# Performance work log

Measured on AMD Instinct MI355X. Metric: run time of the kernel, lower is better.

## Reference

```python
import jax, jax.numpy as jnp
import numpy as np

N_HEADS = 8
HEAD_DIM = 64  # hidden_dim 512 / 8 heads
EPS = 1e-12    # F.normalize clamp_min eps


def setup_inputs() -> dict:
    key = jax.random.key(0)
    k1, k2, k3, k4 = jax.random.split(key, 4)
    B, C, H, W = 2, 256, 48, 48
    hidden = N_HEADS * HEAD_DIM
    x = jax.random.normal(k1, (B, C, H, W), dtype=jnp.float32)
    w_qkv = jax.random.normal(k2, (hidden * 3, C), dtype=jnp.float32) * 0.02
    w_proj = jax.random.normal(k3, (C, hidden), dtype=jnp.float32) * 0.02
    b_proj = jax.random.normal(k4, (C,), dtype=jnp.float32) * 0.02
    return {"x": x, "w_qkv": w_qkv, "w_proj": w_proj, "b_proj": b_proj}


def _l2norm_tokens(t):
    # normalize along the token axis (last dim), matching F.normalize(dim=-1)
    n = jnp.sqrt(jnp.sum(t * t, axis=-1, keepdims=True))
    return t / jnp.maximum(n, EPS)


def reference(x, w_qkv, w_proj, b_proj):
    B, C, H, W = x.shape
    N = H * W
    # 1x1 conv == channel matmul
    qkv = jnp.einsum('oc,bchw->bohw', w_qkv, x)  # [B, 3*hidden, H, W]
    qkv = qkv.reshape(B, 3, N_HEADS, HEAD_DIM, N)
    q, k, v = qkv[:, 0], qkv[:, 1], qkv[:, 2]    # each [B, h, d, N]
    q = _l2norm_tokens(q)
    k = _l2norm_tokens(k)
    # attn = q^T @ k over head_dim -> [B, h, N, N]; note: qk_scale unused in source
    attn = jnp.einsum('bhdn,bhdm->bhnm', q, k)
    attn = jax.nn.softmax(attn, axis=-1)
    # out = attn @ v^T -> [B, h, N, d], then permute to [B, h, d, N]
    out = jnp.einsum('bhnm,bhdm->bhdn', attn, v)
    out = out.reshape(B, N_HEADS * HEAD_DIM, H, W)
    # proj 1x1 conv with bias
    y = jnp.einsum('oc,bchw->bohw', w_proj, out) + b_proj[None, :, None, None]
    return y
```

## Files before the change

### kernel.cpp

```cpp
#include <hip/hip_runtime.h>
#include <math.h>

#define NTOK 2304
#define BATCH 2
#define CIN 256
#define HID 512
#define NH 8
#define LOG2E 1.44269504088896340736f

typedef __attribute__((ext_vector_type(8))) short bfrag;
typedef __attribute__((ext_vector_type(16))) float f32x16;

#if __has_builtin(__builtin_amdgcn_exp2f)
#define EXP2(x) __builtin_amdgcn_exp2f(x)
#else
#define EXP2(x) exp2f(x)
#endif

__device__ __forceinline__ unsigned f2bf(float f) {
    unsigned u = __float_as_uint(f);
    u += 0x7FFF + ((u >> 16) & 1);
    return u >> 16;
}

__device__ __forceinline__ unsigned pk_trunc(float a, float b) {
    return __builtin_amdgcn_perm(__float_as_uint(b), __float_as_uint(a), 0x07060302u);
}

__device__ __forceinline__ void softmax_frag(
    const f32x16& accS, int h, float& ps0, float& ps1, bfrag& P0, bfrag& P1)
{
    unsigned dw[8];
#pragma unroll
    for (int i = 0; i < 8; i++) {
        float plo = EXP2(accS[2 * i]);
        float phi = EXP2(accS[2 * i + 1]);
        dw[i] = pk_trunc(plo, phi);
        ps0 += __uint_as_float(dw[i] << 16);
        ps1 += __uint_as_float(dw[i] & 0xffff0000u);
    }
    unsigned sa0 = h ? dw[0] : dw[2], sb0 = h ? dw[1] : dw[3];
    unsigned sa1 = h ? dw[4] : dw[6], sb1 = h ? dw[5] : dw[7];
    unsigned ra0 = (unsigned)__shfl_xor((int)sa0, 32, 64);
    unsigned rb0 = (unsigned)__shfl_xor((int)sb0, 32, 64);
    unsigned ra1 = (unsigned)__shfl_xor((int)sa1, 32, 64);
    unsigned rb1 = (unsigned)__shfl_xor((int)sb1, 32, 64);
    union { bfrag f; unsigned u[4]; } U0, U1;
    U0.u[0] = h ? ra0 : dw[0];  U0.u[1] = h ? rb0 : dw[1];
    U0.u[2] = h ? dw[2] : ra0;  U0.u[3] = h ? dw[3] : rb0;
    U1.u[0] = h ? ra1 : dw[4];  U1.u[1] = h ? rb1 : dw[5];
    U1.u[2] = h ? dw[6] : ra1;  U1.u[3] = h ? dw[7] : rb1;
    P0 = U0.f; P1 = U1.f;
}

__global__ __launch_bounds__(256) void pack_weights(
    const float* __restrict__ wq, short* __restrict__ wqb,
    const float* __restrict__ wp, short* __restrict__ wpb)
{
    int e = (blockIdx.x * 256 + threadIdx.x) * 8;
    const int NQ = 1536 * 256;
    const float* src; short* dst;
    if (e < NQ) {
        int row = e >> 8, c = e & 255;
        int off = (((row >> 5) * 16 + (c >> 4)) * 64 + ((c >> 3) & 1) * 32 + (row & 31)) * 8;
        src = wq + e; dst = wqb + off;
    } else {
        int e2 = e - NQ;
        int row = e2 >> 9, c = e2 & 511;
        int off = (((row >> 5) * 32 + (c >> 4)) * 64 + ((c >> 3) & 1) * 32 + (row & 31)) * 8;
        src = wp + e2; dst = wpb + off;
    }
    float4 v0 = ((const float4*)src)[0];
    float4 v1 = ((const float4*)src)[1];
    unsigned b0 = f2bf(v0.x) | (f2bf(v0.y) << 16);
    unsigned b1 = f2bf(v0.z) | (f2bf(v0.w) << 16);
    unsigned b2 = f2bf(v1.x) | (f2bf(v1.y) << 16);
    unsigned b3 = f2bf(v1.z) | (f2bf(v1.w) << 16);
    *((uint4*)dst) = make_uint4(b0, b1, b2, b3);
}

__global__ __launch_bounds__(256) void pack_xT(
    const float* __restrict__ x, short* __restrict__ xT)
{
    int n0 = blockIdx.x * 64, c0 = blockIdx.y * 64, b = blockIdx.z;
    __shared__ float sT[64][65];
    int tid = threadIdx.x, lane = tid & 63, wv = tid >> 6;
    for (int c = wv; c < 64; c += 4)
        sT[c][lane] = x[((size_t)b * CIN + c0 + c) * NTOK + n0 + lane];
    __syncthreads();
    int n = tid >> 2, c4 = (tid & 3) * 16;
    unsigned buf[8];
#pragma unroll
    for (int i = 0; i < 8; i++)
        buf[i] = f2bf(sT[c4 + 2 * i][n]) | (f2bf(sT[c4 + 2 * i + 1][n]) << 16);
    int n_tok = n0 + n;
    int l31n = n & 31;
    short* dst = xT + (((size_t)b * 72 + (n_tok >> 5)) * 16 + ((c0 + c4) >> 4)) * 512;
    ((uint4*)(dst + (0 * 32 + l31n) * 8))[0] = make_uint4(buf[0], buf[1], buf[2], buf[3]);
    ((uint4*)(dst + (1 * 32 + l31n) * 8))[0] = make_uint4(buf[4], buf[5], buf[6], buf[7]);
}

__global__ __launch_bounds__(256, 2) void gemm_qkv(
    const short* __restrict__ A,
    const short* __restrict__ B,
    float* __restrict__ qkf, short* __restrict__ vb)
{
    int b = blockIdx.z;
    int o0 = blockIdx.y * 128;
    int n0 = blockIdx.x * 128;
    int tid = threadIdx.x, wv = tid >> 6, lane = tid & 63;
    int h = lane >> 5, l31 = lane & 31;

    const short* pa = A + ((size_t)(o0 >> 5) * 16) * 512 + lane * 8;
    const short* pb = B + (((size_t)b * 72 + (n0 >> 5) + wv) * 16) * 512 + lane * 8;

    f32x16 acc[4];
#pragma unroll
    for (int rb = 0; rb < 4; rb++)
#pragma unroll
        for (int r = 0; r < 16; r++) acc[rb][r] = 0.f;

#pragma unroll 2
    for (int kc = 0; kc < 16; kc++) {
        bfrag a0 = *(const bfrag*)(pa + (size_t)(0 * 16 + kc) * 512);
        bfrag a1 = *(const bfrag*)(pa + (size_t)(1 * 16 + kc) * 512);
        bfrag a2 = *(const bfrag*)(pa + (size_t)(2 * 16 + kc) * 512);
        bfrag a3 = *(const bfrag*)(pa + (size_t)(3 * 16 + kc) * 512);
        bfrag bb = *(const bfrag*)(pb + (size_t)kc * 512);
        acc[0] = __builtin_amdgcn_mfma_f32_32x32x16_bf16(a0, bb, acc[0], 0, 0, 0);
        acc[1] = __builtin_amdgcn_mfma_f32_32x32x16_bf16(a1, bb, acc[1], 0, 0, 0);
        acc[2] = __builtin_amdgcn_mfma_f32_32x32x16_bf16(a2, bb, acc[2], 0, 0, 0);
        acc[3] = __builtin_amdgcn_mfma_f32_32x32x16_bf16(a3, bb, acc[3], 0, 0, 0);
    }

    int nn = n0 + wv * 32 + l31;
    if (o0 < 1024) {
        float* Q = qkf + (size_t)b * 1024 * NTOK;
#pragma unroll
        for (int rb = 0; rb < 4; rb++)
#pragma unroll
            for (int r = 0; r < 16; r++) {
                int ml = (r & 3) + 8 * (r >> 2) + 4 * h;
                Q[(size_t)(o0 + rb * 32 + ml) * NTOK + nn] = acc[rb][r];
            }
    } else {
        short* V = vb + (size_t)b * 512 * NTOK;
        int ov = o0 - 1024;
        int mb = nn >> 5, jc = (nn >> 4) & 1, hv = (nn >> 3) & 1, e = nn & 7;
#pragma unroll
        for (int rb = 0; rb < 4; rb++)
#pragma unroll
            for (int r = 0; r < 16; r++) {
                int ml = (r & 3) + 8 * (r >> 2) + 4 * h;
                int row = ov + rb * 32 + ml;
                int hh2 = row >> 6, dl = row & 63;
                int jr = dl >> 5, l31v = dl & 31;
                V[((((size_t)hh2 * 72 + mb) * 4 + jr * 2 + jc) * 64
                   + hv * 32 + l31v) * 8 + e] = (short)f2bf(acc[rb][r]);
            }
    }
}

__global__ __launch_bounds__(256) void rownorm(
    const float* __restrict__ qkf, float* __restrict__ invn)
{
    int row = blockIdx.x;
    int b = row >> 10, o = row & 1023;
    const float* p = qkf + ((size_t)b * 1024 + o) * NTOK;
    int tid = threadIdx.x;
    float s = 0.f;
    for (int n = tid; n < NTOK; n += 256) { float v = p[n]; s += v * v; }
#pragma unroll
    for (int off = 32; off > 0; off >>= 1) s += __shfl_down(s, off, 64);
    __shared__ float ws[4];
    if ((tid & 63) == 0) ws[tid >> 6] = s;
    __syncthreads();
    if (tid == 0) {
        float tot = ws[0] + ws[1] + ws[2] + ws[3];
        invn[row] = 1.f / fmaxf(sqrtf(tot), 1e-12f);
    }
}

__global__ __launch_bounds__(256) void pack_qk(
    const float* __restrict__ qkf, const float* __restrict__ invn,
    short* __restrict__ qkt)
{
    int n0 = blockIdx.x * 64;
    int bh = blockIdx.y;
    int sel = blockIdx.z;
    int b = bh >> 3, h = bh & 7;
    const float* src = qkf + ((size_t)b * 1024 + sel * 512 + h * 64) * NTOK;
    int base = b * 1024 + sel * 512 + h * 64;
    float extra = sel == 0 ? LOG2E : 1.f;

    __shared__ float sT[64][65];
    int tid = threadIdx.x, lane = tid & 63, wv = tid >> 6;
    for (int d = wv; d < 64; d += 4)
        sT[d][lane] = src[(size_t)d * NTOK + n0 + lane] * (invn[base + d] * extra);
    __syncthreads();

    int n = tid >> 2, c4 = (tid & 3) * 16;
    unsigned buf[8];
#pragma unroll
    for (int i = 0; i < 8; i++)
        buf[i] = f2bf(sT[c4 + 2 * i][n]) | (f2bf(sT[c4 + 2 * i + 1][n]) << 16);
    int t = n0 + n;
    int mb = t >> 5, l31 = t & 31, fi = c4 >> 4;
    short* dst = qkt + (size_t)sel * ((size_t)16 * NTOK * 64)
               + (size_t)bh * NTOK * 64
               + ((size_t)mb * 4 + fi) * 512;
    ((uint4*)(dst + (0 * 32 + l31) * 8))[0] = make_uint4(buf[0], buf[1], buf[2], buf[3]);
    ((uint4*)(dst + (1 * 32 + l31) * 8))[0] = make_uint4(buf[4], buf[5], buf[6], buf[7]);
}

__global__ __launch_bounds__(256, 4) void attn_nb(
    const short* __restrict__ qkt,
    const short* __restrict__ vb,
    float* __restrict__ Opart,
    float* __restrict__ lsum)
{
    int bid = blockIdx.x;
    int g = bid & 31;
    int bh = g >> 1, ms = g & 1;
    int ntile = bid >> 5;
    int b = bh >> 3, hh = bh & 7;
    int tid = threadIdx.x, wv = tid >> 6, lane = tid & 63;
    int h = lane >> 5, l31 = lane & 31;
    int nb = ntile * 128 + wv * 32;
    int mb0 = ms * 36;

    const short* Qt = qkt + (size_t)bh * NTOK * 64;
    const short* kp = qkt + (size_t)16 * NTOK * 64 + (size_t)bh * NTOK * 64
                    + ((size_t)mb0 * 4) * 512 + lane * 8;
    const short* vp = vb + (((size_t)(b * 8 + hh) * 72 + mb0) * 4) * 512 + lane * 8;

    bfrag bQ[4];
    {
        const short* q0 = Qt + ((size_t)(nb >> 5) * 4) * 512 + lane * 8;
#pragma unroll
        for (int i = 0; i < 4; i++) bQ[i] = *(const bfrag*)(q0 + i * 512);
    }

    f32x16 aL, aH;
#pragma unroll
    for (int r = 0; r < 16; r++) { aL[r] = 0.f; aH[r] = 0.f; }
    float s0 = 0.f, s1 = 0.f;

    bfrag ck[4], cv[4];
#pragma unroll
    for (int i = 0; i < 4; i++) {
        ck[i] = *(const bfrag*)(kp + i * 512);
        cv[i] = *(const bfrag*)(vp + i * 512);
    }

#pragma unroll 2
    for (int it = 0; it < 36; it++) {
        kp += 2048; vp += 2048;
        bfrag nk[4], nv[4];
#pragma unroll
        for (int i = 0; i < 4; i++) {
            nk[i] = *(const bfrag*)(kp + i * 512);
            nv[i] = *(const bfrag*)(vp + i * 512);
        }

        bfrag P0, P1;
        {
            f32x16 accS;
#pragma unroll
            for (int r = 0; r < 16; r++) accS[r] = 0.f;
            accS = __builtin_amdgcn_mfma_f32_32x32x16_bf16(ck[0], bQ[0], accS, 0, 0, 0);
            accS = __builtin_amdgcn_mfma_f32_32x32x16_bf16(ck[1], bQ[1], accS, 0, 0, 0);
            accS = __builtin_amdgcn_mfma_f32_32x32x16_bf16(ck[2], bQ[2], accS, 0, 0, 0);
            accS = __builtin_amdgcn_mfma_f32_32x32x16_bf16(ck[3], bQ[3], accS, 0, 0, 0);
            softmax_frag(accS, h, s0, s1, P0, P1);
        }
        aL = __builtin_amdgcn_mfma_f32_32x32x16_bf16(P0, cv[0], aL, 0, 0, 0);
        aL = __builtin_amdgcn_mfma_f32_32x32x16_bf16(P1, cv[1], aL, 0, 0, 0);
        aH = __builtin_amdgcn_mfma_f32_32x32x16_bf16(P0, cv[2], aH, 0, 0, 0);
        aH = __builtin_amdgcn_mfma_f32_32x32x16_bf16(P1, cv[3], aH, 0, 0, 0);

#pragma unroll
        for (int i = 0; i < 4; i++) { ck[i] = nk[i]; cv[i] = nv[i]; }
    }

    float p0 = s0 + s1;
    p0 += __shfl_xor(p0, 32, 64);
    if (h == 0)
        lsum[((size_t)ms * 16 + bh) * NTOK + nb + l31] = p0;

    float* Ob = Opart + (size_t)ms * (2ull * NTOK * HID)
              + (size_t)b * NTOK * HID + hh * 64;
#pragma unroll
    for (int r = 0; r < 16; r++) {
        int ml = (r & 3) + 8 * (r >> 2) + 4 * h;
        Ob[(size_t)(nb + ml) * HID + l31] = aL[r];
        Ob[(size_t)(nb + ml) * HID + 32 + l31] = aH[r];
    }
}

__global__ __launch_bounds__(256) void combine(
    const float* __restrict__ Opart, const float* __restrict__ lsum,
    short* __restrict__ aoT)
{
    int s = blockIdx.x * 256 + threadIdx.x;
    int lane = s & 63, kc = (s >> 6) & 31, nbb = s >> 11;
    int b = nbb >= 72 ? 1 : 0, nb = nbb - 72 * b;
    int h = lane >> 5, l31 = lane & 31;
    int n = nb * 32 + l31;
    int k0 = kc * 16 + h * 8;
    int hh = kc >> 2;
    float l0 = lsum[(size_t)(b * 8 + hh) * NTOK + n];
    float l1 = lsum[(size_t)16 * NTOK + (size_t)(b * 8 + hh) * NTOK + n];
    float inv = 1.f / (l0 + l1);
    const float* P0 = Opart + ((size_t)b * NTOK + n) * HID + k0;
    const float* P1 = P0 + (size_t)2 * NTOK * HID;
    float4 a0 = ((const float4*)P0)[0], a1 = ((const float4*)P0)[1];
    float4 c0 = ((const float4*)P1)[0], c1 = ((const float4*)P1)[1];
    unsigned b0 = f2bf((a0.x + c0.x) * inv) | (f2bf((a0.y + c0.y) * inv) << 16);
    unsigned b1 = f2bf((a0.z + c0.z) * inv) | (f2bf((a0.w + c0.w) * inv) << 16);
    unsigned b2 = f2bf((a1.x + c1.x) * inv) | (f2bf((a1.y + c1.y) * inv) << 16);
    unsigned b3 = f2bf((a1.z + c1.z) * inv) | (f2bf((a1.w + c1.w) * inv) << 16);
    *((uint4*)(aoT + (size_t)s * 8)) = make_uint4(b0, b1, b2, b3);
}

__global__ __launch_bounds__(256, 2) void gemm_proj(
    const short* __restrict__ A,
    const short* __restrict__ B,
    const float* __restrict__ bias, float* __restrict__ y)
{
    int b = blockIdx.z;
    int o0 = blockIdx.y * 64;
    int n0 = blockIdx.x * 128;
    int tid = threadIdx.x, wv = tid >> 6, lane = tid & 63;
    int h = lane >> 5, l31 = lane & 31;

    const short* pa = A + ((size_t)(o0 >> 5) * 32) * 512 + lane * 8;
    const short* pb = B + (((size_t)b * 72 + (n0 >> 5) + wv) * 32) * 512 + lane * 8;

    f32x16 acc0, acc1;
#pragma unroll
    for (int r = 0; r < 16; r++) { acc0[r] = 0.f; acc1[r] = 0.f; }

#pragma unroll 4
    for (int kc = 0; kc < 32; kc++) {
        bfrag a0 = *(const bfrag*)(pa + (size_t)kc * 512);
        bfrag a1 = *(const bfrag*)(pa + (size_t)(32 + kc) * 512);
        bfrag bb = *(const bfrag*)(pb + (size_t)kc * 512);
        acc0 = __builtin_amdgcn_mfma_f32_32x32x16_bf16(a0, bb, acc0, 0, 0, 0);
        acc1 = __builtin_amdgcn_mfma_f32_32x32x16_bf16(a1, bb, acc1, 0, 0, 0);
    }

    int nn = n0 + wv * 32 + l31;
#pragma unroll
    for (int r = 0; r < 16; r++) {
        int ml = (r & 3) + 8 * (r >> 2) + 4 * h;
        y[((size_t)b * CIN + o0 + ml) * NTOK + nn] = acc0[r] + bias[o0 + ml];
        y[((size_t)b * CIN + o0 + 32 + ml) * NTOK + nn] = acc1[r] + bias[o0 + 32 + ml];
    }
}

extern "C" void kernel_launch(void* const* d_in, const int* in_sizes, int n_in,
                              void* d_out, int out_size, void* d_ws, size_t ws_size,
                              hipStream_t stream)
{
    const float* x      = (const float*)d_in[0];
    const float* w_qkv  = (const float*)d_in[1];
    const float* w_proj = (const float*)d_in[2];
    const float* b_proj = (const float*)d_in[3];
    float* y = (float*)d_out;

    float* qkf   = (float*)d_ws;
    float* Opart = (float*)d_ws;
    short* vb    = (short*)((char*)d_ws + 18874368);
    short* qkt   = (short*)((char*)d_ws + 23592960);
    short* aoT   = (short*)((char*)d_ws + 23592960);
    float* lsum  = (float*)((char*)d_ws + 33030144);
    short* xT    = (short*)((char*)d_ws + 33030144);
    short* wqb   = (short*)((char*)d_ws + 35389440);
    short* wpb   = (short*)((char*)d_ws + 36175872);
    float* invn  = (float*)((char*)d_ws + 36438016);

    pack_weights<<<(1536 * 256 + 256 * 512) / 8 / 256, 256, 0, stream>>>(
        w_qkv, wqb, w_proj, wpb);
    pack_xT<<<dim3(NTOK / 64, CIN / 64, BATCH), 256, 0, stream>>>(x, xT);
    gemm_qkv<<<dim3(NTOK / 128, 1536 / 128, BATCH), 256, 0, stream>>>(
        wqb, xT, qkf, vb);
    rownorm<<<2048, 256, 0, stream>>>(qkf, invn);
    pack_qk<<<dim3(NTOK / 64, BATCH * NH, 2), 256, 0, stream>>>(qkf, invn, qkt);
    attn_nb<<<576, 256, 0, stream>>>(qkt, vb, Opart, lsum);
    combine<<<1152, 256, 0, stream>>>(Opart, lsum, aoT);
    gemm_proj<<<dim3(NTOK / 128, CIN / 64, BATCH), 256, 0, stream>>>(
        wpb, aoT, b_proj, y);
}
```

Baseline: 147.5 us.

## Fuse QK norm into GEMM epilogue, split attention keys 4-way with bf16 partials

The QKV GEMM now writes Q/K straight into the packed bf16 attention layout and accumulates per-row sum of squares with atomics. This replaces the fp32 qkf round trip and the separate rownorm and pack_qk kernels with a lightweight in-place scale_qk pass. Attention now splits the key range four ways instead of two, doubling the grid to 1152 blocks. Partial outputs are stored as bf16, which halves partial traffic but costs precision, and combine sums four partials. The trade-offs are atomic contention, a double bf16 rounding on Q/K, and bf16 partial sums.

```diff
diff --git a/kernel.cpp b/kernel.cpp
--- a/kernel.cpp
+++ b/kernel.cpp
@@ -55,8 +55,13 @@
 
 __global__ __launch_bounds__(256) void pack_weights(
     const float* __restrict__ wq, short* __restrict__ wqb,
-    const float* __restrict__ wp, short* __restrict__ wpb)
-{
+    const float* __restrict__ wp, short* __restrict__ wpb,
+    float* __restrict__ sumsq)
+{
+    if (blockIdx.x == 0) {
+        ((float4*)sumsq)[threadIdx.x * 2] = make_float4(0.f, 0.f, 0.f, 0.f);
+        ((float4*)sumsq)[threadIdx.x * 2 + 1] = make_float4(0.f, 0.f, 0.f, 0.f);
+    }
     int e = (blockIdx.x * 256 + threadIdx.x) * 8;
     const int NQ = 1536 * 256;
     const float* src; short* dst;
@@ -103,7 +108,9 @@
 __global__ __launch_bounds__(256, 2) void gemm_qkv(
     const short* __restrict__ A,
     const short* __restrict__ B,
-    float* __restrict__ qkf, short* __restrict__ vb)
+    short* __restrict__ qku,
+    short* __restrict__ vb,
+    float* __restrict__ sumsq)
 {
     int b = blockIdx.z;
     int o0 = blockIdx.y * 128;
@@ -135,13 +142,26 @@
 
     int nn = n0 + wv * 32 + l31;
     if (o0 < 1024) {
-        float* Q = qkf + (size_t)b * 1024 * NTOK;
+        int sel = o0 >> 9;
+        short* Qb = qku + (size_t)sel * (16 * NTOK * 64);
+        int mbase = (nn >> 5) * 4, tl = nn & 31;
 #pragma unroll
         for (int rb = 0; rb < 4; rb++)
 #pragma unroll
             for (int r = 0; r < 16; r++) {
                 int ml = (r & 3) + 8 * (r >> 2) + 4 * h;
-                Q[(size_t)(o0 + rb * 32 + ml) * NTOK + nn] = acc[rb][r];
+                int o = o0 + rb * 32 + ml;
+                int hh2 = (o >> 6) & 7, d = o & 63;
+                float v = acc[rb][r];
+                float sq = v * v;
+#pragma unroll
+                for (int off = 1; off < 32; off <<= 1)
+                    sq += __shfl_xor(sq, off, 64);
+                if (l31 == 0)
+                    atomicAdd(sumsq + b * 1024 + o, sq);
+                Qb[(size_t)(b * 8 + hh2) * (NTOK * 64)
+                   + (size_t)(mbase + (d >> 4)) * 512
+                   + (((d >> 3) & 1) * 32 + tl) * 8 + (d & 7)] = (short)f2bf(v);
             }
     } else {
         short* V = vb + (size_t)b * 512 * NTOK;
@@ -161,73 +181,56 @@
     }
 }
 
-__global__ __launch_bounds__(256) void rownorm(
-    const float* __restrict__ qkf, float* __restrict__ invn)
-{
-    int row = blockIdx.x;
-    int b = row >> 10, o = row & 1023;
-    const float* p = qkf + ((size_t)b * 1024 + o) * NTOK;
-    int tid = threadIdx.x;
-    float s = 0.f;
-    for (int n = tid; n < NTOK; n += 256) { float v = p[n]; s += v * v; }
-#pragma unroll
-    for (int off = 32; off > 0; off >>= 1) s += __shfl_down(s, off, 64);
-    __shared__ float ws[4];
-    if ((tid & 63) == 0) ws[tid >> 6] = s;
-    __syncthreads();
-    if (tid == 0) {
-        float tot = ws[0] + ws[1] + ws[2] + ws[3];
-        invn[row] = 1.f / fmaxf(sqrtf(tot), 1e-12f);
-    }
-}
-
-__global__ __launch_bounds__(256) void pack_qk(
-    const float* __restrict__ qkf, const float* __restrict__ invn,
-    short* __restrict__ qkt)
-{
-    int n0 = blockIdx.x * 64;
-    int bh = blockIdx.y;
-    int sel = blockIdx.z;
-    int b = bh >> 3, h = bh & 7;
-    const float* src = qkf + ((size_t)b * 1024 + sel * 512 + h * 64) * NTOK;
-    int base = b * 1024 + sel * 512 + h * 64;
-    float extra = sel == 0 ? LOG2E : 1.f;
-
-    __shared__ float sT[64][65];
-    int tid = threadIdx.x, lane = tid & 63, wv = tid >> 6;
-    for (int d = wv; d < 64; d += 4)
-        sT[d][lane] = src[(size_t)d * NTOK + n0 + lane] * (invn[base + d] * extra);
-    __syncthreads();
-
-    int n = tid >> 2, c4 = (tid & 3) * 16;
-    unsigned buf[8];
-#pragma unroll
-    for (int i = 0; i < 8; i++)
-        buf[i] = f2bf(sT[c4 + 2 * i][n]) | (f2bf(sT[c4 + 2 * i + 1][n]) << 16);
-    int t = n0 + n;
-    int mb = t >> 5, l31 = t & 31, fi = c4 >> 4;
-    short* dst = qkt + (size_t)sel * ((size_t)16 * NTOK * 64)
-               + (size_t)bh * NTOK * 64
-               + ((size_t)mb * 4 + fi) * 512;
-    ((uint4*)(dst + (0 * 32 + l31) * 8))[0] = make_uint4(buf[0], buf[1], buf[2], buf[3]);
-    ((uint4*)(dst + (1 * 32 + l31) * 8))[0] = make_uint4(buf[4], buf[5], buf[6], buf[7]);
+__global__ __launch_bounds__(256) void scale_qk(
+    short* __restrict__ qkt, const float* __restrict__ sumsq)
+{
+    int s = blockIdx.x * 256 + threadIdx.x;
+    int lane = s & 63;
+    int rest = s >> 6;
+    int fi = rest & 3;
+    int selbh = rest / 288;
+    int sel = selbh >> 4, bh = selbh & 15;
+    int b = bh >> 3, hh = bh & 7;
+    int d0 = fi * 16 + (lane >> 5) * 8;
+    const float* sp = sumsq + b * 1024 + sel * 512 + hh * 64 + d0;
+    float scl = sel == 0 ? LOG2E : 1.f;
+    float4 s0 = ((const float4*)sp)[0];
+    float4 s1 = ((const float4*)sp)[1];
+    float i0 = scl / fmaxf(sqrtf(s0.x), 1e-12f);
+    float i1 = scl / fmaxf(sqrtf(s0.y), 1e-12f);
+    float i2 = scl / fmaxf(sqrtf(s0.z), 1e-12f);
+    float i3 = scl / fmaxf(sqrtf(s0.w), 1e-12f);
+    float i4 = scl / fmaxf(sqrtf(s1.x), 1e-12f);
+    float i5 = scl / fmaxf(sqrtf(s1.y), 1e-12f);
+    float i6 = scl / fmaxf(sqrtf(s1.z), 1e-12f);
+    float i7 = scl / fmaxf(sqrtf(s1.w), 1e-12f);
+    uint4 v = ((uint4*)qkt)[s];
+    unsigned o0w = f2bf(__uint_as_float(v.x << 16) * i0)
+                 | (f2bf(__uint_as_float(v.x & 0xffff0000u) * i1) << 16);
+    unsigned o1w = f2bf(__uint_as_float(v.y << 16) * i2)
+                 | (f2bf(__uint_as_float(v.y & 0xffff0000u) * i3) << 16);
+    unsigned o2w = f2bf(__uint_as_float(v.z << 16) * i4)
+                 | (f2bf(__uint_as_float(v.z & 0xffff0000u) * i5) << 16);
+    unsigned o3w = f2bf(__uint_as_float(v.w << 16) * i6)
+                 | (f2bf(__uint_as_float(v.w & 0xffff0000u) * i7) << 16);
+    ((uint4*)qkt)[s] = make_uint4(o0w, o1w, o2w, o3w);
 }
 
 __global__ __launch_bounds__(256, 4) void attn_nb(
     const short* __restrict__ qkt,
     const short* __restrict__ vb,
-    float* __restrict__ Opart,
+    short* __restrict__ Opart,
     float* __restrict__ lsum)
 {
     int bid = blockIdx.x;
-    int g = bid & 31;
-    int bh = g >> 1, ms = g & 1;
-    int ntile = bid >> 5;
+    int g = bid & 63;
+    int bh = g >> 2, ms = g & 3;
+    int ntile = bid >> 6;
     int b = bh >> 3, hh = bh & 7;
     int tid = threadIdx.x, wv = tid >> 6, lane = tid & 63;
     int h = lane >> 5, l31 = lane & 31;
     int nb = ntile * 128 + wv * 32;
-    int mb0 = ms * 36;
+    int mb0 = ms * 18;
 
     const short* Qt = qkt + (size_t)bh * NTOK * 64;
     const short* kp = qkt + (size_t)16 * NTOK * 64 + (size_t)bh * NTOK * 64
@@ -254,7 +257,7 @@
     }
 
 #pragma unroll 2
-    for (int it = 0; it < 36; it++) {
+    for (int it = 0; it < 18; it++) {
         kp += 2048; vp += 2048;
         bfrag nk[4], nv[4];
 #pragma unroll
@@ -288,18 +291,18 @@
     if (h == 0)
         lsum[((size_t)ms * 16 + bh) * NTOK + nb + l31] = p0;
 
-    float* Ob = Opart + (size_t)ms * (2ull * NTOK * HID)
+    short* Ob = Opart + (size_t)ms * (2ull * NTOK * HID)
               + (size_t)b * NTOK * HID + hh * 64;
 #pragma unroll
     for (int r = 0; r < 16; r++) {
         int ml = (r & 3) + 8 * (r >> 2) + 4 * h;
-        Ob[(size_t)(nb + ml) * HID + l31] = aL[r];
-        Ob[(size_t)(nb + ml) * HID + 32 + l31] = aH[r];
+        Ob[(size_t)(nb + ml) * HID + l31] = (short)f2bf(aL[r]);
+        Ob[(size_t)(nb + ml) * HID + 32 + l31] = (short)f2bf(aH[r]);
     }
 }
 
 __global__ __launch_bounds__(256) void combine(
-    const float* __restrict__ Opart, const float* __restrict__ lsum,
+    const short* __restrict__ Opart, const float* __restrict__ lsum,
     short* __restrict__ aoT)
 {
     int s = blockIdx.x * 256 + threadIdx.x;
@@ -309,17 +312,30 @@
     int n = nb * 32 + l31;
     int k0 = kc * 16 + h * 8;
     int hh = kc >> 2;
-    float l0 = lsum[(size_t)(b * 8 + hh) * NTOK + n];
-    float l1 = lsum[(size_t)16 * NTOK + (size_t)(b * 8 + hh) * NTOK + n];
-    float inv = 1.f / (l0 + l1);
-    const float* P0 = Opart + ((size_t)b * NTOK + n) * HID + k0;
-    const float* P1 = P0 + (size_t)2 * NTOK * HID;
-    float4 a0 = ((const float4*)P0)[0], a1 = ((const float4*)P0)[1];
-    float4 c0 = ((const float4*)P1)[0], c1 = ((const float4*)P1)[1];
-    unsigned b0 = f2bf((a0.x + c0.x) * inv) | (f2bf((a0.y + c0.y) * inv) << 16);
-    unsigned b1 = f2bf((a0.z + c0.z) * inv) | (f2bf((a0.w + c0.w) * inv) << 16);
-    unsigned b2 = f2bf((a1.x + c1.x) * inv) | (f2bf((a1.y + c1.y) * inv) << 16);
-    unsigned b3 = f2bf((a1.z + c1.z) * inv) | (f2bf((a1.w + c1.w) * inv) << 16);
+    float l = 0.f;
+#pragma unroll
+    for (int ms = 0; ms < 4; ms++)
+        l += lsum[((size_t)ms * 16 + b * 8 + hh) * NTOK + n];
+    float inv = 1.f / l;
+    float a[8] = {0.f, 0.f, 0.f, 0.f, 0.f, 0.f, 0.f, 0.f};
+#pragma unroll
+    for (int ms = 0; ms < 4; ms++) {
+        const short* P = Opart + (size_t)ms * (2ull * NTOK * HID)
+                       + ((size_t)b * NTOK + n) * HID + k0;
+        uint4 v = *(const uint4*)P;
+        a[0] += __uint_as_float(v.x << 16);
+        a[1] += __uint_as_float(v.x & 0xffff0000u);
+        a[2] += __uint_as_float(v.y << 16);
+        a[3] += __uint_as_float(v.y & 0xffff0000u);
+        a[4] += __uint_as_float(v.z << 16);
+        a[5] += __uint_as_float(v.z & 0xffff0000u);
+        a[6] += __uint_as_float(v.w << 16);
+        a[7] += __uint_as_float(v.w & 0xffff0000u);
+    }
+    unsigned b0 = f2bf(a[0] * inv) | (f2bf(a[1] * inv) << 16);
+    unsigned b1 = f2bf(a[2] * inv) | (f2bf(a[3] * inv) << 16);
+    unsigned b2 = f2bf(a[4] * inv) | (f2bf(a[5] * inv) << 16);
+    unsigned b3 = f2bf(a[6] * inv) | (f2bf(a[7] * inv) << 16);
     *((uint4*)(aoT + (size_t)s * 8)) = make_uint4(b0, b1, b2, b3);
 }
 
@@ -369,8 +385,7 @@
     const float* b_proj = (const float*)d_in[3];
     float* y = (float*)d_out;
 
-    float* qkf   = (float*)d_ws;
-    float* Opart = (float*)d_ws;
+    short* Opart = (short*)d_ws;
     short* vb    = (short*)((char*)d_ws + 18874368);
     short* qkt   = (short*)((char*)d_ws + 23592960);
     short* aoT   = (short*)((char*)d_ws + 23592960);
@@ -378,16 +393,15 @@
     short* xT    = (short*)((char*)d_ws + 33030144);
     short* wqb   = (short*)((char*)d_ws + 35389440);
     short* wpb   = (short*)((char*)d_ws + 36175872);
-    float* invn  = (float*)((char*)d_ws + 36438016);
+    float* sumsq = (float*)((char*)d_ws + 36438016);
 
     pack_weights<<<(1536 * 256 + 256 * 512) / 8 / 256, 256, 0, stream>>>(
-        w_qkv, wqb, w_proj, wpb);
+        w_qkv, wqb, w_proj, wpb, sumsq);
     pack_xT<<<dim3(NTOK / 64, CIN / 64, BATCH), 256, 0, stream>>>(x, xT);
     gemm_qkv<<<dim3(NTOK / 128, 1536 / 128, BATCH), 256, 0, stream>>>(
-        wqb, xT, qkf, vb);
-    rownorm<<<2048, 256, 0, stream>>>(qkf, invn);
-    pack_qk<<<dim3(NTOK / 64, BATCH * NH, 2), 256, 0, stream>>>(qkf, invn, qkt);
-    attn_nb<<<576, 256, 0, stream>>>(qkt, vb, Opart, lsum);
+        wqb, xT, qkt, vb, sumsq);
+    scale_qk<<<2304, 256, 0, stream>>>(qkt, sumsq);
+    attn_nb<<<1152, 256, 0, stream>>>(qkt, vb, Opart, lsum);
     combine<<<1152, 256, 0, stream>>>(Opart, lsum, aoT);
     gemm_proj<<<dim3(NTOK / 128, CIN / 64, BATCH), 256, 0, stream>>>(
         wpb, aoT, b_proj, y);
```

Result: slower. 163.0 us (+10.5%).
